# Optimization experiments

Measured on AMD Instinct MI355X. Metric: run time of the kernel, lower is better.

## Reference

```python
import jax, jax.numpy as jnp
import numpy as np

N = 50000      # nodes
E = 800000     # edges (before self-loops)
G = 256        # graphs in batch
IN = 64        # in_dim
H = 8          # n_heads
C = 16         # gat_dim (per-head out channels)
HID = 128      # decoder hidden
OUT = H * C    # 128 = concat GAT output = graph_embedding_dim
NEG_SLOPE = 0.2


def setup_inputs() -> dict:
    key = jax.random.key(0)
    ks = jax.random.split(key, 12)
    op_features = jax.random.normal(ks[0], (N, IN), dtype=jnp.float32)
    edge_index = jax.random.randint(ks[1], (2, E), 0, N, dtype=jnp.int64)
    batch_index = jnp.sort(jax.random.randint(ks[2], (N,), 0, G, dtype=jnp.int64))
    # GATConv params (PyG: lin weight, att_src, att_dst, bias)
    W_gat = jax.random.normal(ks[3], (IN, H * C), dtype=jnp.float32) / np.sqrt(IN)
    att_src = jax.random.normal(ks[4], (H, C), dtype=jnp.float32) / np.sqrt(C)
    att_dst = jax.random.normal(ks[5], (H, C), dtype=jnp.float32) / np.sqrt(C)
    bias_gat = jnp.zeros((H * C,), dtype=jnp.float32)
    # Decoder MLP: Linear(OUT+OUT, 128) -> ReLU -> Linear(128, 1)
    W1 = jax.random.normal(ks[6], (2 * OUT, HID), dtype=jnp.float32) / np.sqrt(2 * OUT)
    b1 = jnp.zeros((HID,), dtype=jnp.float32)
    W2 = jax.random.normal(ks[7], (HID, 1), dtype=jnp.float32) / np.sqrt(HID)
    b2 = jnp.zeros((1,), dtype=jnp.float32)
    return {
        "op_features": op_features, "edge_index": edge_index, "batch_index": batch_index,
        "W_gat": W_gat, "att_src": att_src, "att_dst": att_dst, "bias_gat": bias_gat,
        "W1": W1, "b1": b1, "W2": W2, "b2": b2,
    }


def _gat_conv(x_in, src, dst, W_gat, att_src, att_dst, bias_gat):
    # x: [N, H, C] transformed node features
    x = (x_in @ W_gat).reshape(N, H, C)
    # per-node attention logits (PyG splits alpha into src+dst halves)
    a_src = jnp.einsum('nhc,hc->nh', x, att_src)   # [N, H]
    a_dst = jnp.einsum('nhc,hc->nh', x, att_dst)   # [N, H]
    # edge logits: message flows src -> dst
    alpha = jax.nn.leaky_relu(a_src[src] + a_dst[dst], NEG_SLOPE)  # [E', H]
    # scatter-softmax over incoming edges of each dst node
    m = jax.ops.segment_max(alpha, dst, num_segments=N)            # [N, H]
    e = jnp.exp(alpha - m[dst])                                    # [E', H]
    s = jax.ops.segment_sum(e, dst, num_segments=N)                # [N, H]
    a = e / s[dst]
    # weighted aggregation of source features
    out = jax.ops.segment_sum(a[:, :, None] * x[src], dst, num_segments=N)  # [N, H, C]
    return out.reshape(N, H * C) + bias_gat


def reference(op_features, edge_index, batch_index, W_gat, att_src, att_dst,
              bias_gat, W1, b1, W2, b2):
    # add self-loops (PyG GATConv default add_self_loops=True)
    loop = jnp.arange(N, dtype=edge_index.dtype)
    src = jnp.concatenate([edge_index[0], loop])
    dst = jnp.concatenate([edge_index[1], loop])

    op_embedding = jax.nn.elu(_gat_conv(op_features, src, dst,
                                        W_gat, att_src, att_dst, bias_gat))  # [N, OUT]
    # global_mean_pool
    sums = jax.ops.segment_sum(op_embedding, batch_index, num_segments=G)    # [G, OUT]
    cnts = jax.ops.segment_sum(jnp.ones((N,), op_embedding.dtype), batch_index, num_segments=G)
    graph_embedding = sums / jnp.maximum(cnts, 1.0)[:, None]
    # gather-broadcast + concat + MLP decoder
    combined = jnp.concatenate([op_embedding, graph_embedding[batch_index]], axis=1)  # [N, 2*OUT]
    h = jax.nn.relu(combined @ W1 + b1)
    scores = (h @ W2 + b2).squeeze(-1)   # [N]
    return scores, graph_embedding
```

## Files before the change

### kernel.cpp

```cpp
#include <hip/hip_runtime.h>
#include <hip/hip_bf16.h>
#include <hip/hip_fp16.h>

constexpr int N_   = 50000;
constexpr int E_   = 800000;
constexpr int G_   = 256;
constexpr int IN_  = 64;
constexpr int H_   = 8;
constexpr int OUT_ = 128;
constexpr float NEG_SLOPE = 0.2f;
constexpr int NBUCK = (N_ + 255) / 256;
constexpr int EPB   = 2048;
constexpr int NBINB = (E_ + EPB - 1) / EPB;
constexpr int CAP   = 6144;
constexpr int NXF   = (N_ + 63) / 64;

typedef _Float16 f16x8 __attribute__((ext_vector_type(8)));
typedef float    f32x4 __attribute__((ext_vector_type(4)));

constexpr size_t OFF_X      = 0;
constexpr size_t OFF_EMBH   = OFF_X      + (size_t)N_*OUT_*2;
constexpr size_t OFF_ASRC   = OFF_X      + (size_t)N_*OUT_*4;
constexpr size_t OFF_ADST   = OFF_ASRC   + (size_t)N_*H_*4;
constexpr size_t OFF_PAIRS  = OFF_ADST   + (size_t)N_*H_*4;
constexpr size_t OFF_BCNT   = OFF_PAIRS  + (size_t)NBUCK*CAP*4;
constexpr size_t OFF_WT     = OFF_BCNT   + 1024;
constexpr size_t OFF_WP     = OFF_WT     + 128*128*2;
constexpr size_t OFF_ROWS   = OFF_WP     + 18432;
constexpr size_t OFF_EIDX   = OFF_ROWS   + 200448;
constexpr size_t OFF_GPART  = OFF_EIDX   + (size_t)E_*4;
constexpr size_t OFF_GSUM   = OFF_GPART  + (size_t)G_*OUT_*4;

__global__ void k_prep(const float* __restrict__ Wg, const float* __restrict__ att_s,
                       const float* __restrict__ att_d, const float* __restrict__ W1,
                       __half* __restrict__ wp, __half* __restrict__ wt,
                       int* __restrict__ bcnt, float* __restrict__ gsum) {
    const int b = blockIdx.x, t = threadIdx.x;
    if (b == 0) {
        for (int i = t; i < NBUCK; i += 256) bcnt[i] = 0;
        for (int idx = t; idx < 16 * 64; idx += 256) {
            int jp = idx >> 6, k = idx & 63;
            int h = jp & 7;
            const float* att = (jp < 8) ? att_s : att_d;
            float s = 0.f;
#pragma unroll
            for (int c = 0; c < 16; ++c)
                s = fmaf(Wg[k * 128 + h * 16 + c], att[h * 16 + c], s);
            wp[(128 + jp) * 64 + k] = __float2half(s);
        }
    } else if (b <= 8) {
        for (int idx = t; idx < 1024; idx += 256) {
            int e = (b - 1) * 1024 + idx;
            int j = e >> 6, k = e & 63;
            wp[j * 64 + k] = __float2half(Wg[k * 128 + j]);
        }
    } else {
        for (int idx = t; idx < 2048; idx += 256) {
            int e = (b - 9) * 2048 + idx;
            int j = e >> 7, k = e & 127;
            wt[j * 128 + k] = __float2half(W1[(size_t)k * 128 + j]);
        }
        for (int idx = t; idx < 4096; idx += 256)
            gsum[(size_t)(b - 9) * 4096 + idx] = 0.f;
    }
}

__global__ __launch_bounds__(256) void k_binx(const int* __restrict__ src,
                                              const int* __restrict__ dst,
                                              int* __restrict__ bcnt,
                                              unsigned int* __restrict__ pairs,
                                              const float* __restrict__ feat,
                                              const __half* __restrict__ wp,
                                              __half* __restrict__ xh,
                                              float* __restrict__ asrc,
                                              float* __restrict__ adst) {
    union SMem {
        struct { int cnt[NBUCK]; int base[NBUCK]; } bin;
        struct { _Float16 fs[64][64]; _Float16 wp_s[144][64]; } xf;
    };
    __shared__ SMem sm;
    const int tid = threadIdx.x;

    if (blockIdx.x < NBINB) {
        int* cnt  = sm.bin.cnt;
        int* base = sm.bin.base;
        for (int i = tid; i < NBUCK; i += 256) cnt[i] = 0;
        __syncthreads();
        const int e0 = blockIdx.x * EPB;
        const int ne = min(EPB, E_ - e0);
        for (int i = tid; i < ne; i += 256) atomicAdd(&cnt[dst[e0 + i] >> 8], 1);
        __syncthreads();
        for (int i = tid; i < NBUCK; i += 256) {
            int c = cnt[i];
            base[i] = (c > 0) ? atomicAdd(&bcnt[i], c) : 0;
            cnt[i] = 0;
        }
        __syncthreads();
        for (int i = tid; i < ne; i += 256) {
            int d = dst[e0 + i];
            int s = src[e0 + i];
            int b = d >> 8;
            int p = base[b] + atomicAdd(&cnt[b], 1);
            pairs[(size_t)b * CAP + p] = ((unsigned int)(d & 255) << 16) | (unsigned int)s;
        }
        return;
    }

    const int base = (blockIdx.x - NBINB) * 64;
    for (int c = tid; c < 1152; c += 256) {
        int j = c >> 3, kk = (c & 7) * 8;
        *(float4*)&sm.xf.wp_s[j][kk] = *(const float4*)&wp[j * 64 + kk];
    }
    for (int c = tid; c < 512; c += 256) {
        int nl = c >> 3, kk = (c & 7) * 8;
        int n = base + nl;
        _Float16 h8[8];
        if (n < N_) {
            float4 f0 = *(const float4*)&feat[(size_t)n * 64 + kk];
            float4 f1 = *(const float4*)&feat[(size_t)n * 64 + kk + 4];
            h8[0]=(_Float16)f0.x; h8[1]=(_Float16)f0.y; h8[2]=(_Float16)f0.z; h8[3]=(_Float16)f0.w;
            h8[4]=(_Float16)f1.x; h8[5]=(_Float16)f1.y; h8[6]=(_Float16)f1.z; h8[7]=(_Float16)f1.w;
        } else {
#pragma unroll
            for (int q = 0; q < 8; ++q) h8[q] = (_Float16)0.f;
        }
        *(float4*)&sm.xf.fs[nl][kk] = *(float4*)h8;
    }
    __syncthreads();

    const int wv   = tid >> 6;
    const int lane = tid & 63;
    const int rc   = lane & 15;
    const int kh   = lane >> 4;

    f32x4 acc[9];
#pragma unroll
    for (int nt = 0; nt < 9; ++nt) acc[nt] = (f32x4){0.f, 0.f, 0.f, 0.f};

#pragma unroll
    for (int kt = 0; kt < 2; ++kt) {
        f16x8 a = *(const f16x8*)&sm.xf.fs[wv * 16 + rc][kt * 32 + kh * 8];
#pragma unroll
        for (int nt = 0; nt < 9; ++nt) {
            f16x8 bfr = *(const f16x8*)&sm.xf.wp_s[nt * 16 + rc][kt * 32 + kh * 8];
            acc[nt] = __builtin_amdgcn_mfma_f32_16x16x32_f16(a, bfr, acc[nt], 0, 0, 0);
        }
    }

#pragma unroll
    for (int r = 0; r < 4; ++r) {
        int n = base + wv * 16 + kh * 4 + r;
        if (n >= N_) continue;
#pragma unroll
        for (int nt = 0; nt < 8; ++nt)
            xh[(size_t)n * OUT_ + nt * 16 + rc] = __float2half(acc[nt][r]);
        if (rc < 8) asrc[n * H_ + rc] = acc[8][r];
        else        adst[n * H_ + (rc - 8)] = acc[8][r];
    }
}

__global__ __launch_bounds__(256) void k_scat3(const unsigned int* __restrict__ pairs,
                                               const int* __restrict__ bcnt,
                                               int* __restrict__ rowstart,
                                               int* __restrict__ eidx) {
    __shared__ int sh[256];
    __shared__ int h0[256];
    __shared__ int h1[256];
    __shared__ int cur[256];
    const int b    = blockIdx.x >> 1;
    const int half = blockIdx.x & 1;
    const int t    = threadIdx.x;

    int v0 = (t < NBUCK) ? bcnt[t] : 0;
    sh[t] = v0;
    __syncthreads();
    for (int off = 1; off < 256; off <<= 1) {
        int u = (t >= off) ? sh[t - off] : 0;
        __syncthreads();
        sh[t] += u;
        __syncthreads();
    }
    const int bstart_b = (b == 0) ? 0 : sh[b - 1];
    const int nb = bcnt[b];
    const int nh = nb >> 1;
    __syncthreads();

    h0[t] = 0;
    h1[t] = 0;
    __syncthreads();
    const size_t p0 = (size_t)b * CAP;
    for (int i = t; i < nh; i += 256) atomicAdd(&h0[pairs[p0 + i] >> 16], 1);
    for (int i = nh + t; i < nb; i += 256) atomicAdd(&h1[pairs[p0 + i] >> 16], 1);
    __syncthreads();
    int v = h0[t] + h1[t];
    sh[t] = v;
    __syncthreads();
    for (int off = 1; off < 256; off <<= 1) {
        int u = (t >= off) ? sh[t - off] : 0;
        __syncthreads();
        sh[t] += u;
        __syncthreads();
    }
    int rs = bstart_b + sh[t] - v;
    if (half == 0) {
        int n = b * 256 + t;
        if (n < N_) rowstart[n] = rs;
        if (b == NBUCK - 1 && t == 0) rowstart[N_] = E_;
    }
    cur[t] = rs + (half ? h0[t] : 0);
    __syncthreads();
    const int ibeg = half ? nh : 0;
    const int iend = half ? nb : nh;
    for (int i = ibeg + t; i < iend; i += 256) {
        unsigned int pk = pairs[p0 + i];
        int pos = atomicAdd(&cur[pk >> 16], 1);
        eidx[pos] = (int)(pk & 0xFFFFu);
    }
}

__global__ void k_agg(const int* __restrict__ rowstart, const int* __restrict__ eidx,
                      const __half* __restrict__ xh, const float* __restrict__ asrc,
                      const float* __restrict__ adst, const float* __restrict__ bias,
                      const int* __restrict__ batch, float* __restrict__ gsum,
                      __half* __restrict__ embh) {
    const int wvi  = threadIdx.x >> 6;
    const int dn   = blockIdx.x * 4 + wvi;
    const int lane = threadIdx.x & 63;
    const int h    = lane >> 3;
    const float adst_h = adst[dn * H_ + h];
    const uint choff = (uint)lane * 2;

    const int beg = rowstart[dn];
    const int end = rowstart[dn + 1];

    float ax = 0.f, ay = 0.f, sw = 0.f;
    int i = beg;
    for (; i + 7 < end; i += 8) {
        int s0 = eidx[i];
        int s1 = eidx[i + 1];
        int s2 = eidx[i + 2];
        int s3 = eidx[i + 3];
        int s4 = eidx[i + 4];
        int s5 = eidx[i + 5];
        int s6 = eidx[i + 6];
        int s7 = eidx[i + 7];
        __half2 x0 = *(const __half2*)(xh + ((uint)s0 * OUT_ + choff));
        __half2 x1 = *(const __half2*)(xh + ((uint)s1 * OUT_ + choff));
        __half2 x2 = *(const __half2*)(xh + ((uint)s2 * OUT_ + choff));
        __half2 x3 = *(const __half2*)(xh + ((uint)s3 * OUT_ + choff));
        __half2 x4 = *(const __half2*)(xh + ((uint)s4 * OUT_ + choff));
        __half2 x5 = *(const __half2*)(xh + ((uint)s5 * OUT_ + choff));
        __half2 x6 = *(const __half2*)(xh + ((uint)s6 * OUT_ + choff));
        __half2 x7 = *(const __half2*)(xh + ((uint)s7 * OUT_ + choff));
        float a0 = asrc[(uint)s0 * H_ + h] + adst_h;
        float a1 = asrc[(uint)s1 * H_ + h] + adst_h;
        float a2 = asrc[(uint)s2 * H_ + h] + adst_h;
        float a3 = asrc[(uint)s3 * H_ + h] + adst_h;
        float a4 = asrc[(uint)s4 * H_ + h] + adst_h;
        float a5 = asrc[(uint)s5 * H_ + h] + adst_h;
        float a6 = asrc[(uint)s6 * H_ + h] + adst_h;
        float a7 = asrc[(uint)s7 * H_ + h] + adst_h;
        a0 = (a0 > 0.f) ? a0 : NEG_SLOPE * a0;
        a1 = (a1 > 0.f) ? a1 : NEG_SLOPE * a1;
        a2 = (a2 > 0.f) ? a2 : NEG_SLOPE * a2;
        a3 = (a3 > 0.f) ? a3 : NEG_SLOPE * a3;
        a4 = (a4 > 0.f) ? a4 : NEG_SLOPE * a4;
        a5 = (a5 > 0.f) ? a5 : NEG_SLOPE * a5;
        a6 = (a6 > 0.f) ? a6 : NEG_SLOPE * a6;
        a7 = (a7 > 0.f) ? a7 : NEG_SLOPE * a7;
        float w0 = __expf(a0);
        float w1 = __expf(a1);
        float w2 = __expf(a2);
        float w3 = __expf(a3);
        float w4 = __expf(a4);
        float w5 = __expf(a5);
        float w6 = __expf(a6);
        float w7 = __expf(a7);
        float2 f0 = __half22float2(x0);
        float2 f1 = __half22float2(x1);
        float2 f2 = __half22float2(x2);
        float2 f3 = __half22float2(x3);
        float2 f4 = __half22float2(x4);
        float2 f5 = __half22float2(x5);
        float2 f6 = __half22float2(x6);
        float2 f7 = __half22float2(x7);
        ax = fmaf(w0, f0.x, fmaf(w1, f1.x, fmaf(w2, f2.x, fmaf(w3, f3.x, ax))));
        ax = fmaf(w4, f4.x, fmaf(w5, f5.x, fmaf(w6, f6.x, fmaf(w7, f7.x, ax))));
        ay = fmaf(w0, f0.y, fmaf(w1, f1.y, fmaf(w2, f2.y, fmaf(w3, f3.y, ay))));
        ay = fmaf(w4, f4.y, fmaf(w5, f5.y, fmaf(w6, f6.y, fmaf(w7, f7.y, ay))));
        sw += ((w0 + w1) + (w2 + w3)) + ((w4 + w5) + (w6 + w7));
    }
    for (; i + 3 < end; i += 4) {
        int s0 = eidx[i];
        int s1 = eidx[i + 1];
        int s2 = eidx[i + 2];
        int s3 = eidx[i + 3];
        __half2 x0 = *(const __half2*)(xh + ((uint)s0 * OUT_ + choff));
        __half2 x1 = *(const __half2*)(xh + ((uint)s1 * OUT_ + choff));
        __half2 x2 = *(const __half2*)(xh + ((uint)s2 * OUT_ + choff));
        __half2 x3 = *(const __half2*)(xh + ((uint)s3 * OUT_ + choff));
        float a0 = asrc[(uint)s0 * H_ + h] + adst_h;
        float a1 = asrc[(uint)s1 * H_ + h] + adst_h;
        float a2 = asrc[(uint)s2 * H_ + h] + adst_h;
        float a3 = asrc[(uint)s3 * H_ + h] + adst_h;
        a0 = (a0 > 0.f) ? a0 : NEG_SLOPE * a0;
        a1 = (a1 > 0.f) ? a1 : NEG_SLOPE * a1;
        a2 = (a2 > 0.f) ? a2 : NEG_SLOPE * a2;
        a3 = (a3 > 0.f) ? a3 : NEG_SLOPE * a3;
        float w0 = __expf(a0);
        float w1 = __expf(a1);
        float w2 = __expf(a2);
        float w3 = __expf(a3);
        float2 f0 = __half22float2(x0);
        float2 f1 = __half22float2(x1);
        float2 f2 = __half22float2(x2);
        float2 f3 = __half22float2(x3);
        ax = fmaf(w0, f0.x, fmaf(w1, f1.x, fmaf(w2, f2.x, fmaf(w3, f3.x, ax))));
        ay = fmaf(w0, f0.y, fmaf(w1, f1.y, fmaf(w2, f2.y, fmaf(w3, f3.y, ay))));
        sw += (w0 + w1) + (w2 + w3);
    }
    for (; i < end; ++i) {
        int s0 = eidx[i];
        __half2 x0 = *(const __half2*)(xh + ((uint)s0 * OUT_ + choff));
        float a0 = asrc[(uint)s0 * H_ + h] + adst_h;
        a0 = (a0 > 0.f) ? a0 : NEG_SLOPE * a0;
        float w0 = __expf(a0);
        float2 f0 = __half22float2(x0);
        ax = fmaf(w0, f0.x, ax);
        ay = fmaf(w0, f0.y, ay);
        sw += w0;
    }
    {
        float al = asrc[(uint)dn * H_ + h] + adst_h;
        al = (al > 0.f) ? al : NEG_SLOPE * al;
        float w = __expf(al);
        __half2 xv = *(const __half2*)(xh + ((uint)dn * OUT_ + choff));
        float2 fv = __half22float2(xv);
        ax = fmaf(w, fv.x, ax);
        ay = fmaf(w, fv.y, ay);
        sw += w;
    }
    float ox = ax / sw + bias[lane * 2];
    float oy = ay / sw + bias[lane * 2 + 1];
    ox = (ox > 0.f) ? ox : expm1f(ox);
    oy = (oy > 0.f) ? oy : expm1f(oy);
    *(__half2*)&embh[(size_t)dn * OUT_ + lane * 2] = __floats2half2_rn(ox, oy);

    __shared__ float px[4][64];
    __shared__ float py[4][64];
    __shared__ int   gidv[4];
    px[wvi][lane] = ox;
    py[wvi][lane] = oy;
    if (lane == 0) gidv[wvi] = batch[dn];
    __syncthreads();
    if (wvi == 0) {
        float sx = px[0][lane], sy = py[0][lane];
        int gc = gidv[0];
#pragma unroll
        for (int w = 1; w < 4; ++w) {
            if (gidv[w] == gc) {
                sx += px[w][lane];
                sy += py[w][lane];
            } else {
                unsafeAtomicAdd(&gsum[gc * OUT_ + lane * 2], sx);
                unsafeAtomicAdd(&gsum[gc * OUT_ + lane * 2 + 1], sy);
                gc = gidv[w];
                sx = px[w][lane];
                sy = py[w][lane];
            }
        }
        unsafeAtomicAdd(&gsum[gc * OUT_ + lane * 2], sx);
        unsafeAtomicAdd(&gsum[gc * OUT_ + lane * 2 + 1], sy);
    }
}

__global__ void k_graph(const int* __restrict__ batch, const float* __restrict__ gsum,
                        const float* __restrict__ W1, const float* __restrict__ b1,
                        float* __restrict__ outg, float* __restrict__ gpart) {
    const int g = blockIdx.x;
    const int j = threadIdx.x;
    __shared__ float ge[128];
    __shared__ int cnt_s;
    if (j == 0) {
        int lo = 0, hi = N_;
        while (lo < hi) { int m = (lo + hi) >> 1; if (batch[m] < g) lo = m + 1; else hi = m; }
        int start = lo;
        lo = 0; hi = N_;
        while (lo < hi) { int m = (lo + hi) >> 1; if (batch[m] <= g) lo = m + 1; else hi = m; }
        cnt_s = lo - start;
    }
    __syncthreads();
    float v = gsum[g * 128 + j] / fmaxf((float)cnt_s, 1.f);
    ge[j] = v;
    outg[g * 128 + j] = v;
    __syncthreads();
    float s = b1[j];
    const float* w = W1 + (size_t)128 * 128 + j;
    for (int k = 0; k < 128; ++k) s = fmaf(ge[k], w[(size_t)k * 128], s);
    gpart[g * 128 + j] = s;
}

__global__ __launch_bounds__(256) void k_dec3(const __half* __restrict__ embh,
                                              const __half* __restrict__ wtg,
                                              const float* __restrict__ gpart,
                                              const int* __restrict__ batch,
                                              const float* __restrict__ W2,
                                              const float* __restrict__ b2,
                                              float* __restrict__ scores) {
    __shared__ _Float16 wt_s[128][128];
    __shared__ _Float16 emb_s[64][128];
    __shared__ float    w2_s[128];
    const int base = blockIdx.x * 64;
    const int tid  = threadIdx.x;

    for (int c = tid; c < 2048; c += 256) {
        int j = c >> 4, kk = (c & 15) * 8;
        *(float4*)&wt_s[j][kk] = *(const float4*)&wtg[j * 128 + kk];
    }
    for (int c = tid; c < 1024; c += 256) {
        int nl = c >> 4, kk = (c & 15) * 8;
        int n = base + nl;
        if (n < N_)
            *(float4*)&emb_s[nl][kk] = *(const float4*)&embh[(size_t)n * 128 + kk];
        else
            *(float4*)&emb_s[nl][kk] = make_float4(0.f, 0.f, 0.f, 0.f);
    }
    if (tid < 128) w2_s[tid] = W2[tid];
    __syncthreads();

    const int wv   = tid >> 6;
    const int lane = tid & 63;
    const int rc   = lane & 15;
    const int kh   = lane >> 4;

    f32x4 acc[8];
#pragma unroll
    for (int nt = 0; nt < 8; ++nt) acc[nt] = (f32x4){0.f, 0.f, 0.f, 0.f};

#pragma unroll
    for (int kt = 0; kt < 4; ++kt) {
        f16x8 a = *(const f16x8*)&emb_s[wv * 16 + rc][kt * 32 + kh * 8];
#pragma unroll
        for (int nt = 0; nt < 8; ++nt) {
            f16x8 bfr = *(const f16x8*)&wt_s[nt * 16 + rc][kt * 32 + kh * 8];
            acc[nt] = __builtin_amdgcn_mfma_f32_16x16x32_f16(a, bfr, acc[nt], 0, 0, 0);
        }
    }

    const float b2v = b2[0];
    float s[4] = {0.f, 0.f, 0.f, 0.f};
    int   gi[4];
#pragma unroll
    for (int r = 0; r < 4; ++r) {
        int n = base + wv * 16 + kh * 4 + r;
        gi[r] = (n < N_) ? batch[n] : 0;
    }
#pragma unroll
    for (int nt = 0; nt < 8; ++nt) {
        int j = nt * 16 + rc;
        float w2 = w2_s[j];
#pragma unroll
        for (int r = 0; r < 4; ++r) {
            float hv = acc[nt][r] + gpart[(size_t)gi[r] * 128 + j];
            hv = (hv > 0.f) ? hv : 0.f;
            s[r] = fmaf(hv, w2, s[r]);
        }
    }
#pragma unroll
    for (int r = 0; r < 4; ++r) {
#pragma unroll
        for (int m = 8; m >= 1; m >>= 1) s[r] += __shfl_xor(s[r], m, 16);
    }
    if (rc == 0) {
#pragma unroll
        for (int r = 0; r < 4; ++r) {
            int n = base + wv * 16 + kh * 4 + r;
            if (n < N_) scores[n] = s[r] + b2v;
        }
    }
}

extern "C" void kernel_launch(void* const* d_in, const int* in_sizes, int n_in,
                              void* d_out, int out_size, void* d_ws, size_t ws_size,
                              hipStream_t stream) {
    const float* feat   = (const float*)d_in[0];
    const int*   ei     = (const int*)d_in[1];
    const int*   batch  = (const int*)d_in[2];
    const float* Wg     = (const float*)d_in[3];
    const float* att_s  = (const float*)d_in[4];
    const float* att_d  = (const float*)d_in[5];
    const float* bias_g = (const float*)d_in[6];
    const float* W1     = (const float*)d_in[7];
    const float* b1     = (const float*)d_in[8];
    const float* W2     = (const float*)d_in[9];
    const float* b2     = (const float*)d_in[10];
    char*  wsb = (char*)d_ws;
    float* out = (float*)d_out;

    const int* src = ei;
    const int* dst = ei + E_;

    __half* XH    = (__half*)(wsb + OFF_X);
    __half* EMBH  = (__half*)(wsb + OFF_EMBH);
    float*  ASRC  = (float*)(wsb + OFF_ASRC);
    float*  ADST  = (float*)(wsb + OFF_ADST);
    unsigned int* PAIRS = (unsigned int*)(wsb + OFF_PAIRS);
    int*    BCNT  = (int*)  (wsb + OFF_BCNT);
    __half* WT    = (__half*)(wsb + OFF_WT);
    __half* WP    = (__half*)(wsb + OFF_WP);
    int*    ROWS  = (int*)  (wsb + OFF_ROWS);
    int*    EIDX  = (int*)  (wsb + OFF_EIDX);
    float*  GPART = (float*)(wsb + OFF_GPART);
    float*  GSUM  = (float*)(wsb + OFF_GSUM);

    k_prep<<<17, 256, 0, stream>>>(Wg, att_s, att_d, W1, WP, WT, BCNT, GSUM);
    k_binx<<<NBINB + NXF, 256, 0, stream>>>(src, dst, BCNT, PAIRS,
                                            feat, WP, XH, ASRC, ADST);
    k_scat3<<<2 * NBUCK, 256, 0, stream>>>(PAIRS, BCNT, ROWS, EIDX);
    k_agg<<<N_ / 4, 256, 0, stream>>>(ROWS, EIDX, XH, ASRC, ADST, bias_g,
                                      batch, GSUM, EMBH);
    k_graph<<<G_, 128, 0, stream>>>(batch, GSUM, W1, b1, out + N_, GPART);
    k_dec3<<<(N_ + 63) / 64, 256, 0, stream>>>(EMBH, WT, GPART, batch, W2, b2, out);
}
```

Measured before the change: 120.6 us.

## Precompute per-edge attention weights during CSR scatter and read them in aggregation

Per-edge exp(leaky_relu(a_src+a_dst)) weights for all 8 heads are now computed once in the scatter kernel and stored as fp16 in CSR order. The aggregation kernel loads these weights contiguously instead of gathering asrc per edge and evaluating exp in every lane. The intent is to cut redundant transcendental work and random asrc gathers in the hot aggregation loop. In exchange it adds an extra 800K×16-byte write and read, moves work into the scatter kernel, drops the 4-wide remainder loop, and stores weights in fp16, which costs precision.

New measurement: 135.5 us. 1.12x slower.

```diff
diff --git a/kernel.cpp b/kernel.cpp
--- a/kernel.cpp
+++ b/kernel.cpp
@@ -30,6 +30,7 @@
 constexpr size_t OFF_EIDX   = OFF_ROWS   + 200448;
 constexpr size_t OFF_GPART  = OFF_EIDX   + (size_t)E_*4;
 constexpr size_t OFF_GSUM   = OFF_GPART  + (size_t)G_*OUT_*4;
+constexpr size_t OFF_EWT    = OFF_GSUM   + (size_t)G_*OUT_*4;
 
 __global__ void k_prep(const float* __restrict__ Wg, const float* __restrict__ att_s,
                        const float* __restrict__ att_d, const float* __restrict__ W1,
@@ -161,12 +162,16 @@
 
 __global__ __launch_bounds__(256) void k_scat3(const unsigned int* __restrict__ pairs,
                                                const int* __restrict__ bcnt,
+                                               const float* __restrict__ asrc,
+                                               const float* __restrict__ adst,
                                                int* __restrict__ rowstart,
-                                               int* __restrict__ eidx) {
+                                               int* __restrict__ eidx,
+                                               __half* __restrict__ ewt) {
     __shared__ int sh[256];
     __shared__ int h0[256];
     __shared__ int h1[256];
     __shared__ int cur[256];
+    __shared__ float ads[256][8];
     const int b    = blockIdx.x >> 1;
     const int half = blockIdx.x & 1;
     const int t    = threadIdx.x;
@@ -187,6 +192,15 @@
 
     h0[t] = 0;
     h1[t] = 0;
+    {
+        int n = b * 256 + t;
+        if (n < N_) {
+            float4 a0 = *(const float4*)&adst[(size_t)n * 8];
+            float4 a1 = *(const float4*)&adst[(size_t)n * 8 + 4];
+            *(float4*)&ads[t][0] = a0;
+            *(float4*)&ads[t][4] = a1;
+        }
+    }
     __syncthreads();
     const size_t p0 = (size_t)b * CAP;
     for (int i = t; i < nh; i += 256) atomicAdd(&h0[pairs[p0 + i] >> 16], 1);
@@ -213,21 +227,33 @@
     const int iend = half ? nb : nh;
     for (int i = ibeg + t; i < iend; i += 256) {
         unsigned int pk = pairs[p0 + i];
-        int pos = atomicAdd(&cur[pk >> 16], 1);
-        eidx[pos] = (int)(pk & 0xFFFFu);
+        int d = (int)(pk >> 16);
+        int s = (int)(pk & 0xFFFFu);
+        int pos = atomicAdd(&cur[d], 1);
+        eidx[pos] = s;
+        float4 a0 = *(const float4*)&asrc[(size_t)s * 8];
+        float4 a1 = *(const float4*)&asrc[(size_t)s * 8 + 4];
+        float av[8] = {a0.x, a0.y, a0.z, a0.w, a1.x, a1.y, a1.z, a1.w};
+        __half wv8[8];
+#pragma unroll
+        for (int h = 0; h < 8; ++h) {
+            float al = av[h] + ads[d][h];
+            al = (al > 0.f) ? al : NEG_SLOPE * al;
+            wv8[h] = __float2half(__expf(al));
+        }
+        *(float4*)&ewt[(size_t)pos * 8] = *(float4*)wv8;
     }
 }
 
 __global__ void k_agg(const int* __restrict__ rowstart, const int* __restrict__ eidx,
-                      const __half* __restrict__ xh, const float* __restrict__ asrc,
-                      const float* __restrict__ adst, const float* __restrict__ bias,
-                      const int* __restrict__ batch, float* __restrict__ gsum,
-                      __half* __restrict__ embh) {
+                      const __half* __restrict__ ewt, const __half* __restrict__ xh,
+                      const float* __restrict__ asrc, const float* __restrict__ adst,
+                      const float* __restrict__ bias, const int* __restrict__ batch,
+                      float* __restrict__ gsum, __half* __restrict__ embh) {
     const int wvi  = threadIdx.x >> 6;
     const int dn   = blockIdx.x * 4 + wvi;
     const int lane = threadIdx.x & 63;
     const int h    = lane >> 3;
-    const float adst_h = adst[dn * H_ + h];
     const uint choff = (uint)lane * 2;
 
     const int beg = rowstart[dn];
@@ -252,30 +278,14 @@
         __half2 x5 = *(const __half2*)(xh + ((uint)s5 * OUT_ + choff));
         __half2 x6 = *(const __half2*)(xh + ((uint)s6 * OUT_ + choff));
         __half2 x7 = *(const __half2*)(xh + ((uint)s7 * OUT_ + choff));
-        float a0 = asrc[(uint)s0 * H_ + h] + adst_h;
-        float a1 = asrc[(uint)s1 * H_ + h] + adst_h;
-        float a2 = asrc[(uint)s2 * H_ + h] + adst_h;
-        float a3 = asrc[(uint)s3 * H_ + h] + adst_h;
-        float a4 = asrc[(uint)s4 * H_ + h] + adst_h;
-        float a5 = asrc[(uint)s5 * H_ + h] + adst_h;
-        float a6 = asrc[(uint)s6 * H_ + h] + adst_h;
-        float a7 = asrc[(uint)s7 * H_ + h] + adst_h;
-        a0 = (a0 > 0.f) ? a0 : NEG_SLOPE * a0;
-        a1 = (a1 > 0.f) ? a1 : NEG_SLOPE * a1;
-        a2 = (a2 > 0.f) ? a2 : NEG_SLOPE * a2;
-        a3 = (a3 > 0.f) ? a3 : NEG_SLOPE * a3;
-        a4 = (a4 > 0.f) ? a4 : NEG_SLOPE * a4;
-        a5 = (a5 > 0.f) ? a5 : NEG_SLOPE * a5;
-        a6 = (a6 > 0.f) ? a6 : NEG_SLOPE * a6;
-        a7 = (a7 > 0.f) ? a7 : NEG_SLOPE * a7;
-        float w0 = __expf(a0);
-        float w1 = __expf(a1);
-        float w2 = __expf(a2);
-        float w3 = __expf(a3);
-        float w4 = __expf(a4);
-        float w5 = __expf(a5);
-        float w6 = __expf(a6);
-        float w7 = __expf(a7);
+        float w0 = __half2float(ewt[(size_t)(i + 0) * 8 + h]);
+        float w1 = __half2float(ewt[(size_t)(i + 1) * 8 + h]);
+        float w2 = __half2float(ewt[(size_t)(i + 2) * 8 + h]);
+        float w3 = __half2float(ewt[(size_t)(i + 3) * 8 + h]);
+        float w4 = __half2float(ewt[(size_t)(i + 4) * 8 + h]);
+        float w5 = __half2float(ewt[(size_t)(i + 5) * 8 + h]);
+        float w6 = __half2float(ewt[(size_t)(i + 6) * 8 + h]);
+        float w7 = __half2float(ewt[(size_t)(i + 7) * 8 + h]);
         float2 f0 = __half22float2(x0);
         float2 f1 = __half22float2(x1);
         float2 f2 = __half22float2(x2);
@@ -290,48 +300,17 @@
         ay = fmaf(w4, f4.y, fmaf(w5, f5.y, fmaf(w6, f6.y, fmaf(w7, f7.y, ay))));
         sw += ((w0 + w1) + (w2 + w3)) + ((w4 + w5) + (w6 + w7));
     }
-    for (; i + 3 < end; i += 4) {
-        int s0 = eidx[i];
-        int s1 = eidx[i + 1];
-        int s2 = eidx[i + 2];
-        int s3 = eidx[i + 3];
-        __half2 x0 = *(const __half2*)(xh + ((uint)s0 * OUT_ + choff));
-        __half2 x1 = *(const __half2*)(xh + ((uint)s1 * OUT_ + choff));
-        __half2 x2 = *(const __half2*)(xh + ((uint)s2 * OUT_ + choff));
-        __half2 x3 = *(const __half2*)(xh + ((uint)s3 * OUT_ + choff));
-        float a0 = asrc[(uint)s0 * H_ + h] + adst_h;
-        float a1 = asrc[(uint)s1 * H_ + h] + adst_h;
-        float a2 = asrc[(uint)s2 * H_ + h] + adst_h;
-        float a3 = asrc[(uint)s3 * H_ + h] + adst_h;
-        a0 = (a0 > 0.f) ? a0 : NEG_SLOPE * a0;
-        a1 = (a1 > 0.f) ? a1 : NEG_SLOPE * a1;
-        a2 = (a2 > 0.f) ? a2 : NEG_SLOPE * a2;
-        a3 = (a3 > 0.f) ? a3 : NEG_SLOPE * a3;
-        float w0 = __expf(a0);
-        float w1 = __expf(a1);
-        float w2 = __expf(a2);
-        float w3 = __expf(a3);
-        float2 f0 = __half22float2(x0);
-        float2 f1 = __half22float2(x1);
-        float2 f2 = __half22float2(x2);
-        float2 f3 = __half22float2(x3);
-        ax = fmaf(w0, f0.x, fmaf(w1, f1.x, fmaf(w2, f2.x, fmaf(w3, f3.x, ax))));
-        ay = fmaf(w0, f0.y, fmaf(w1, f1.y, fmaf(w2, f2.y, fmaf(w3, f3.y, ay))));
-        sw += (w0 + w1) + (w2 + w3);
-    }
     for (; i < end; ++i) {
         int s0 = eidx[i];
         __half2 x0 = *(const __half2*)(xh + ((uint)s0 * OUT_ + choff));
-        float a0 = asrc[(uint)s0 * H_ + h] + adst_h;
-        a0 = (a0 > 0.f) ? a0 : NEG_SLOPE * a0;
-        float w0 = __expf(a0);
+        float w0 = __half2float(ewt[(size_t)i * 8 + h]);
         float2 f0 = __half22float2(x0);
         ax = fmaf(w0, f0.x, ax);
         ay = fmaf(w0, f0.y, ay);
         sw += w0;
     }
     {
-        float al = asrc[(uint)dn * H_ + h] + adst_h;
+        float al = asrc[(uint)dn * H_ + h] + adst[(uint)dn * H_ + h];
         al = (al > 0.f) ? al : NEG_SLOPE * al;
         float w = __expf(al);
         __half2 xv = *(const __half2*)(xh + ((uint)dn * OUT_ + choff));
@@ -512,12 +491,13 @@
     int*    EIDX  = (int*)  (wsb + OFF_EIDX);
     float*  GPART = (float*)(wsb + OFF_GPART);
     float*  GSUM  = (float*)(wsb + OFF_GSUM);
+    __half* EWT   = (__half*)(wsb + OFF_EWT);
 
     k_prep<<<17, 256, 0, stream>>>(Wg, att_s, att_d, W1, WP, WT, BCNT, GSUM);
     k_binx<<<NBINB + NXF, 256, 0, stream>>>(src, dst, BCNT, PAIRS,
                                             feat, WP, XH, ASRC, ADST);
-    k_scat3<<<2 * NBUCK, 256, 0, stream>>>(PAIRS, BCNT, ROWS, EIDX);
-    k_agg<<<N_ / 4, 256, 0, stream>>>(ROWS, EIDX, XH, ASRC, ADST, bias_g,
+    k_scat3<<<2 * NBUCK, 256, 0, stream>>>(PAIRS, BCNT, ASRC, ADST, ROWS, EIDX, EWT);
+    k_agg<<<N_ / 4, 256, 0, stream>>>(ROWS, EIDX, EWT, XH, ASRC, ADST, bias_g,
                                       batch, GSUM, EMBH);
     k_graph<<<G_, 128, 0, stream>>>(batch, GSUM, W1, b1, out + N_, GPART);
     k_dec3<<<(N_ + 63) / 64, 256, 0, stream>>>(EMBH, WT, GPART, batch, W2, b2, out);
```
